# Kernel optimization log

Measured on AMD Instinct MI355X. Metric: run time of the kernel, lower is better.

Reference implementation:

```python
import jax, jax.numpy as jnp
import numpy as np

K = 3          # kernel_size
STRIDE = 1
BLOCK = 64     # block_size
OUT_FEATURES = 512
IN_CH = 256
IN_FEATURES = K * K * IN_CH          # 2304
Q = IN_FEATURES // BLOCK             # 36 (exact)
P = OUT_FEATURES // BLOCK            # 8


def _unfold(x, k, stride):
    # torch F.unfold with padding=k//2: output (B, C*k*k, Ho*Wo),
    # feature order channel-major then (di, dj)
    B, C, H, W = x.shape
    pad = k // 2
    xp = jnp.pad(x, ((0, 0), (0, 0), (pad, pad), (pad, pad)))
    Ho = (H + 2 * pad - k) // stride + 1
    Wo = (W + 2 * pad - k) // stride + 1
    cols = jnp.stack(
        [xp[:, :, di:di + (Ho - 1) * stride + 1:stride,
                  dj:dj + (Wo - 1) * stride + 1:stride]
         for di in range(k) for dj in range(k)],
        axis=2)  # (B, C, k*k, Ho, Wo)
    return cols.reshape(B, C * k * k, Ho * Wo), Ho, Wo


def setup_inputs() -> dict:
    key = jax.random.key(0)
    k1, k2 = jax.random.split(key)
    x = jax.random.normal(k1, (8, IN_CH, 32, 32), dtype=jnp.float32)
    # xavier-uniform-like init on (p, q, block)
    fan_in, fan_out = Q * BLOCK, P * BLOCK
    a = float(np.sqrt(6.0 / (fan_in + fan_out)))
    weight = jax.random.uniform(k2, (P, Q, BLOCK), dtype=jnp.float32,
                                minval=-a, maxval=a)
    return {"x": x, "weight": weight}


def reference(x, weight):
    B = x.shape[0]
    H = x.shape[2]
    xu, Ho, Wo = _unfold(x, K, STRIDE)          # (B, in_features, L)
    pad_rows = Q * BLOCK - IN_FEATURES          # 0 here, kept for faithfulness
    xu = jnp.pad(xu, ((0, 0), (0, pad_rows), (0, 0)))
    # faithful to torch reshape semantics (row-major over (B, q*b, L))
    xb = xu.reshape(-1, Q, BLOCK)               # (N, q, b), N = B*L
    xf = jnp.fft.rfft(xb)                       # (N, q, bf)
    wf = jnp.fft.rfft(weight)                   # (p, q, bf)
    hf = jnp.sum(xf[:, None, :, :] * wf[None, :, :, :], axis=2)  # (N, p, bf)
    h = jnp.fft.irfft(hf, n=BLOCK)              # (N, p, b)
    h = h.reshape(-1, P * BLOCK)
    if P * BLOCK > OUT_FEATURES:
        h = h[:, :OUT_FEATURES]
    L = (H // STRIDE) * (H // STRIDE)
    h = h.reshape(B, L, OUT_FEATURES)
    h = jnp.transpose(h, (0, 2, 1))
    return h.reshape(B, OUT_FEATURES, H // STRIDE, H // STRIDE)
```

## Files before the change

### kernel.cpp

```cpp
#include <hip/hip_runtime.h>
#include <hip/hip_bf16.h>


#define QK 2304
#define MROWS 8192
#define NOC 512
#define QB 36

typedef __attribute__((ext_vector_type(8))) short short8;
typedef __attribute__((ext_vector_type(4))) float floatx4;

__device__ __forceinline__ ushort f2bf(float f) {
    __hip_bfloat16 h = __float2bfloat16(f);
    return *reinterpret_cast<ushort*>(&h);
}

__device__ __forceinline__ void async16(const void* g, void* l) {
    __builtin_amdgcn_global_load_lds((const __attribute__((address_space(1))) void*)g,
                                     (__attribute__((address_space(3))) void*)l, 16, 0, 0);
}

#define PREP_A_BLOCKS 2048
#define PREP_B_BLOCKS 576

__global__ __launch_bounds__(256) void bcc_prep(const float* __restrict__ x,
                                                const float* __restrict__ w,
                                                ushort* __restrict__ wsA,
                                                ushort* __restrict__ wsB) {
    if (blockIdx.x < PREP_A_BLOCKS) {
        __shared__ float img[1024];
        const int bb = blockIdx.x >> 8, c = blockIdx.x & 255;
        const float* src = x + ((size_t)bb * 256 + c) * 1024;
        *(float4*)&img[threadIdx.x * 4] = *(const float4*)&src[threadIdx.x * 4];
        __syncthreads();

        const int loc0 = threadIdx.x * 4;
        ushort* dstbase = wsA + ((size_t)bb * 2304 + c * 9) * 1024 + loc0;
        #pragma unroll
        for (int kk = 0; kk < 9; ++kk) {
            const int di = kk / 3, dj = kk - di * 3;
            const int off = (di - 1) * 32 + (dj - 1);
            const bool row_ok = (unsigned)((loc0 >> 5) + di - 1) < 32u;
            ushort u[4];
            #pragma unroll
            for (int e = 0; e < 4; ++e) {
                int wi = ((loc0 + e) & 31) + dj - 1;
                bool ok = row_ok && ((unsigned)wi < 32u);
                float v = ok ? img[loc0 + e + off] : 0.f;
                u[e] = f2bf(v);
            }
            *(ushort4*)&dstbase[(size_t)kk * 1024] = make_ushort4(u[0], u[1], u[2], u[3]);
        }
    } else {
        int t = (blockIdx.x - PREP_A_BLOCKS) * 256 + threadIdx.x;
        int n = t / 288;
        int o = t - n * 288;
        int p = n >> 6, tt = n & 63;
        int k0 = o * 8;
        ushort u[8];
        #pragma unroll
        for (int e = 0; e < 8; ++e) {
            int k = k0 + e;
            int q = k >> 6, s = k & 63;
            u[e] = f2bf(w[(p * QB + q) * 64 + ((tt - s) & 63)]);
        }
        *(ushort4*)&wsB[(size_t)n * QK + k0]     = make_ushort4(u[0], u[1], u[2], u[3]);
        *(ushort4*)&wsB[(size_t)n * QK + k0 + 4] = make_ushort4(u[4], u[5], u[6], u[7]);
    }
}

__global__ __launch_bounds__(512) void bcc_mfma(const ushort* __restrict__ A,
                                                const ushort* __restrict__ Bm,
                                                float* __restrict__ out) {
    __shared__ ushort smem[3][2][128 * 64];

    const int tid = threadIdx.x;
    const int l = tid & 63, w = tid >> 6;
    const int t3 = w & 3, ks = w >> 2;
    const int wm = t3 & 1, wn = t3 >> 1;

    const int lin = blockIdx.x;
    const int n_idx = (lin >> 3) & 3;
    const int m_idx = ((lin >> 5) << 3) | (lin & 7);
    const int n0 = n_idx * 128;
    const int m0 = m_idx * 128;
    const int b  = m0 >> 10, r0 = m0 & 1023;

    const int lr = l & 15, lq = l >> 4;
    const int lrow = l >> 3;
    const int lkoff = ((l & 7) ^ (lrow & 7)) * 8;

    floatx4 acc[4][4];
    #pragma unroll
    for (int i = 0; i < 4; ++i)
        #pragma unroll
        for (int j = 0; j < 4; ++j) acc[i][j] = (floatx4){0.f, 0.f, 0.f, 0.f};

    auto stage = [&](int q, int buf) {
        const int kb = q * 64;
        #pragma unroll
        for (int t = 0; t < 2; ++t) {
            int row8 = w * 16 + t * 8;
            async16(A  + ((size_t)(m0 + row8 + lrow) * QK + kb + lkoff),
                    &smem[buf][0][row8 * 64]);
            async16(Bm + ((size_t)(n0 + row8 + lrow) * QK + kb + lkoff),
                    &smem[buf][1][row8 * 64]);
        }
    };

    stage(0, 0);
    stage(1, 1);
    const int ca = ks * 4 + lq;
    for (int q = 0; q < QB; ++q) {
        const int buf = q % 3;
        if (q + 2 < QB) {
            stage(q + 2, (q + 2) % 3);
            asm volatile("s_waitcnt vmcnt(8)" ::: "memory");
        } else if (q + 1 < QB) {
            asm volatile("s_waitcnt vmcnt(4)" ::: "memory");
        } else {
            asm volatile("s_waitcnt vmcnt(0)" ::: "memory");
        }
        __builtin_amdgcn_s_barrier();
        asm volatile("" ::: "memory");

        short8 av[4], bv[4];
        #pragma unroll
        for (int i = 0; i < 4; ++i) {
            int Ra = wm * 64 + i * 16 + lr;
            av[i] = *(const short8*)&smem[buf][0][Ra * 64 + ((ca ^ (Ra & 7)) * 8)];
        }
        #pragma unroll
        for (int j = 0; j < 4; ++j) {
            int Rb = wn * 64 + j * 16 + lr;
            bv[j] = *(const short8*)&smem[buf][1][Rb * 64 + ((ca ^ (Rb & 7)) * 8)];
        }
        #pragma unroll
        for (int i = 0; i < 4; ++i)
            #pragma unroll
            for (int j = 0; j < 4; ++j)
                acc[i][j] = __builtin_amdgcn_mfma_f32_16x16x32_bf16(bv[j], av[i], acc[i][j], 0, 0, 0);

        asm volatile("" ::: "memory");
        __builtin_amdgcn_s_barrier();
    }

    float* fsm = (float*)&smem[0][0][0];
    __syncthreads();
    if (ks == 1) {
        #pragma unroll
        for (int i = 0; i < 4; ++i)
            #pragma unroll
            for (int j = 0; j < 4; ++j)
                *(floatx4*)&fsm[t3 * 4096 + (i * 4 + j) * 256 + l * 4] = acc[i][j];
    }
    __syncthreads();
    if (ks == 0) {
        #pragma unroll
        for (int i = 0; i < 4; ++i)
            #pragma unroll
            for (int j = 0; j < 4; ++j) {
                floatx4 o4 = *(const floatx4*)&fsm[t3 * 4096 + (i * 4 + j) * 256 + l * 4];
                #pragma unroll
                for (int e = 0; e < 4; ++e) acc[i][j][e] += o4[e];
            }
    }
    __syncthreads();
    if (ks == 0) {
        #pragma unroll
        for (int i = 0; i < 4; ++i) {
            int rl = wm * 64 + i * 16 + lr;
            #pragma unroll
            for (int j = 0; j < 4; ++j) {
                int ocl0 = wn * 64 + j * 16 + lq * 4;
                #pragma unroll
                for (int e = 0; e < 4; ++e)
                    fsm[(ocl0 + e) * 132 + rl] = acc[i][j][e];
            }
        }
    }
    __syncthreads();
    {
        float* outb = out + ((size_t)b * NOC + n0) * 1024 + r0;
        #pragma unroll
        for (int rr = 0; rr < 16; ++rr) {
            int ocl = w * 16 + rr;
            float2 v = *(const float2*)&fsm[ocl * 132 + l * 2];
            *(float2*)&outb[(size_t)ocl * 1024 + l * 2] = v;
        }
    }
}

__global__ __launch_bounds__(256) void bcc_gemm_f32(
    const float* __restrict__ x, const float* __restrict__ w,
    float* __restrict__ out) {
    __shared__ float Asf[64][68];
    __shared__ float Wsf[64][68];
    const int tid = threadIdx.x;
    const int tn = tid & 15, tm = tid >> 4;
    const int p = blockIdx.x;
    const int m0 = blockIdx.y * 64;
    const int b = m0 >> 10, r0 = m0 & 1023;
    const float* xb = x + (size_t)b * (256 * 32 * 32);
    float acc[4][4] = {};
    for (int q = 0; q < QB; ++q) {
        #pragma unroll
        for (int i = 0; i < 16; ++i) {
            int idx = i * 256 + tid;
            int s = idx & 63, mm = idx >> 6;
            int flat = (r0 + mm) * QK + q * 64 + s;
            int feat = flat >> 10, loc = flat & 1023;
            int c = feat / 9, kk = feat - c * 9;
            int hi = (loc >> 5) + (kk / 3) - 1;
            int wi = (loc & 31) + (kk % 3) - 1;
            float v = 0.0f;
            if ((unsigned)hi < 32u && (unsigned)wi < 32u)
                v = xb[(c * 32 + hi) * 32 + wi];
            Asf[mm][s] = v;
        }
        const float* wb = w + (p * QB + q) * 64;
        #pragma unroll
        for (int i = 0; i < 16; ++i) {
            int idx = i * 256 + tid;
            int t = idx & 63, s = idx >> 6;
            Wsf[s][t] = wb[(t - s) & 63];
        }
        __syncthreads();
        #pragma unroll
        for (int s0 = 0; s0 < 64; s0 += 4) {
            float4 a4[4], b4[4];
            #pragma unroll
            for (int i2 = 0; i2 < 4; ++i2)
                a4[i2] = *(const float4*)&Asf[tm * 4 + i2][s0];
            #pragma unroll
            for (int ss = 0; ss < 4; ++ss)
                b4[ss] = *(const float4*)&Wsf[s0 + ss][tn * 4];
            #pragma unroll
            for (int i2 = 0; i2 < 4; ++i2) {
                const float* av = (const float*)&a4[i2];
                #pragma unroll
                for (int ss = 0; ss < 4; ++ss) {
                    float a = av[ss];
                    acc[i2][0] += a * b4[ss].x;
                    acc[i2][1] += a * b4[ss].y;
                    acc[i2][2] += a * b4[ss].z;
                    acc[i2][3] += a * b4[ss].w;
                }
            }
        }
        __syncthreads();
    }
    float* outb = out + (size_t)b * NOC * 1024;
    const int r_base = r0 + tm * 4;
    #pragma unroll
    for (int j = 0; j < 4; ++j) {
        int oc = p * 64 + tn * 4 + j;
        float4 v = make_float4(acc[0][j], acc[1][j], acc[2][j], acc[3][j]);
        *(float4*)&outb[(size_t)oc * 1024 + r_base] = v;
    }
}

extern "C" void kernel_launch(void* const* d_in, const int* in_sizes, int n_in,
                              void* d_out, int out_size, void* d_ws, size_t ws_size,
                              hipStream_t stream) {
    const float* x = (const float*)d_in[0];
    const float* w = (const float*)d_in[1];
    float* out = (float*)d_out;

    const size_t bytesA = (size_t)MROWS * QK * sizeof(ushort);
    const size_t bytesB = (size_t)NOC * QK * sizeof(ushort);

    if (ws_size >= bytesA + bytesB) {
        ushort* wsA = (ushort*)d_ws;
        ushort* wsB = (ushort*)((char*)d_ws + bytesA);
        bcc_prep<<<PREP_A_BLOCKS + PREP_B_BLOCKS, 256, 0, stream>>>(x, w, wsA, wsB);
        bcc_mfma<<<256, 512, 0, stream>>>(wsA, wsB, out);
    } else {
        bcc_gemm_f32<<<dim3(8, MROWS / 64), 256, 0, stream>>>(x, w, out);
    }
}
```

Baseline: 95.93 us.

## Double K tile to 128 with double buffering instead of triple buffering

The MFMA GEMM main loop now stages 128-wide K chunks (18 iterations instead of 36) using two LDS buffers in place of three 64-wide buffers. The swizzle widens to 16 chunks per row, and each wave issues two MFMA k-steps per iteration. This halves the number of barriers and loop overheads. In exchange, prefetch depth drops to one stage ahead and the LDS footprint grows (128 KB), which may reduce occupancy and latency hiding.

```diff
diff --git a/kernel.cpp b/kernel.cpp
--- a/kernel.cpp
+++ b/kernel.cpp
@@ -5,7 +5,7 @@
 #define QK 2304
 #define MROWS 8192
 #define NOC 512
-#define QB 36
+#define QB 18
 
 typedef __attribute__((ext_vector_type(8))) short short8;
 typedef __attribute__((ext_vector_type(4))) float floatx4;
@@ -62,7 +62,7 @@
         for (int e = 0; e < 8; ++e) {
             int k = k0 + e;
             int q = k >> 6, s = k & 63;
-            u[e] = f2bf(w[(p * QB + q) * 64 + ((tt - s) & 63)]);
+            u[e] = f2bf(w[(p * 36 + q) * 64 + ((tt - s) & 63)]);
         }
         *(ushort4*)&wsB[(size_t)n * QK + k0]     = make_ushort4(u[0], u[1], u[2], u[3]);
         *(ushort4*)&wsB[(size_t)n * QK + k0 + 4] = make_ushort4(u[4], u[5], u[6], u[7]);
@@ -72,7 +72,7 @@
 __global__ __launch_bounds__(512) void bcc_mfma(const ushort* __restrict__ A,
                                                 const ushort* __restrict__ Bm,
                                                 float* __restrict__ out) {
-    __shared__ ushort smem[3][2][128 * 64];
+    __shared__ ushort smem[2][2][128 * 128];
 
     const int tid = threadIdx.x;
     const int l = tid & 63, w = tid >> 6;
@@ -87,8 +87,8 @@
     const int b  = m0 >> 10, r0 = m0 & 1023;
 
     const int lr = l & 15, lq = l >> 4;
-    const int lrow = l >> 3;
-    const int lkoff = ((l & 7) ^ (lrow & 7)) * 8;
+    const int srow = l >> 4;
+    const int schunk = l & 15;
 
     floatx4 acc[4][4];
     #pragma unroll
@@ -97,49 +97,57 @@
         for (int j = 0; j < 4; ++j) acc[i][j] = (floatx4){0.f, 0.f, 0.f, 0.f};
 
     auto stage = [&](int q, int buf) {
-        const int kb = q * 64;
-        #pragma unroll
-        for (int t = 0; t < 2; ++t) {
-            int row8 = w * 16 + t * 8;
-            async16(A  + ((size_t)(m0 + row8 + lrow) * QK + kb + lkoff),
-                    &smem[buf][0][row8 * 64]);
-            async16(Bm + ((size_t)(n0 + row8 + lrow) * QK + kb + lkoff),
-                    &smem[buf][1][row8 * 64]);
+        const int kb = q * 128;
+        #pragma unroll
+        for (int t = 0; t < 4; ++t) {
+            int row4 = w * 16 + t * 4;
+            int row  = row4 + srow;
+            int ch   = schunk ^ (row & 15);
+            async16(A  + ((size_t)(m0 + row) * QK + kb + ch * 8),
+                    &smem[buf][0][row4 * 128]);
+            async16(Bm + ((size_t)(n0 + row) * QK + kb + ch * 8),
+                    &smem[buf][1][row4 * 128]);
         }
     };
 
     stage(0, 0);
-    stage(1, 1);
-    const int ca = ks * 4 + lq;
     for (int q = 0; q < QB; ++q) {
-        const int buf = q % 3;
-        if (q + 2 < QB) {
-            stage(q + 2, (q + 2) % 3);
+        const int buf = q & 1;
+        if (q + 1 < QB) {
+            stage(q + 1, buf ^ 1);
             asm volatile("s_waitcnt vmcnt(8)" ::: "memory");
-        } else if (q + 1 < QB) {
-            asm volatile("s_waitcnt vmcnt(4)" ::: "memory");
         } else {
             asm volatile("s_waitcnt vmcnt(0)" ::: "memory");
         }
         __builtin_amdgcn_s_barrier();
         asm volatile("" ::: "memory");
 
-        short8 av[4], bv[4];
+        short8 av[4][2], bv[4][2];
         #pragma unroll
         for (int i = 0; i < 4; ++i) {
             int Ra = wm * 64 + i * 16 + lr;
-            av[i] = *(const short8*)&smem[buf][0][Ra * 64 + ((ca ^ (Ra & 7)) * 8)];
+            #pragma unroll
+            for (int s = 0; s < 2; ++s) {
+                int ca = (ks * 2 + s) * 4 + lq;
+                av[i][s] = *(const short8*)&smem[buf][0][Ra * 128 + ((ca ^ (Ra & 15)) * 8)];
+            }
         }
         #pragma unroll
         for (int j = 0; j < 4; ++j) {
             int Rb = wn * 64 + j * 16 + lr;
-            bv[j] = *(const short8*)&smem[buf][1][Rb * 64 + ((ca ^ (Rb & 7)) * 8)];
-        }
-        #pragma unroll
-        for (int i = 0; i < 4; ++i)
-            #pragma unroll
-            for (int j = 0; j < 4; ++j)
-                acc[i][j] = __builtin_amdgcn_mfma_f32_16x16x32_bf16(bv[j], av[i], acc[i][j], 0, 0, 0);
+            #pragma unroll
+            for (int s = 0; s < 2; ++s) {
+                int ca = (ks * 2 + s) * 4 + lq;
+                bv[j][s] = *(const short8*)&smem[buf][1][Rb * 128 + ((ca ^ (Rb & 15)) * 8)];
+            }
+        }
+        #pragma unroll
+        for (int s = 0; s < 2; ++s)
+            #pragma unroll
+            for (int i = 0; i < 4; ++i)
+                #pragma unroll
+                for (int j = 0; j < 4; ++j)
+                    acc[i][j] = __builtin_amdgcn_mfma_f32_16x16x32_bf16(bv[j][s], av[i][s], acc[i][j], 0, 0, 0);
 
         asm volatile("" ::: "memory");
         __builtin_amdgcn_s_barrier();
@@ -203,7 +211,7 @@
     const int b = m0 >> 10, r0 = m0 & 1023;
     const float* xb = x + (size_t)b * (256 * 32 * 32);
     float acc[4][4] = {};
-    for (int q = 0; q < QB; ++q) {
+    for (int q = 0; q < 36; ++q) {
         #pragma unroll
         for (int i = 0; i < 16; ++i) {
             int idx = i * 256 + tid;
@@ -218,7 +226,7 @@
                 v = xb[(c * 32 + hi) * 32 + wi];
             Asf[mm][s] = v;
         }
-        const float* wb = w + (p * QB + q) * 64;
+        const float* wb = w + (p * 36 + q) * 64;
         #pragma unroll
         for (int i = 0; i < 16; ++i) {
             int idx = i * 256 + tid;
```

After: 96.27 us. No clear change (+0.4%).
